# Kernel tuning notes

Measured on AMD Instinct MI355X. Metric: run time of the kernel, lower is better.

The kernel has to match this reference:

```python
import jax, jax.numpy as jnp
import numpy as np

B, S, Nv, D, DF, H = 8, 1024, 768, 512, 2048, 8
DH = D // H
EPS = 1e-5


def _layernorm(x, g, b):
    mu = jnp.mean(x, axis=-1, keepdims=True)
    var = jnp.mean((x - mu) ** 2, axis=-1, keepdims=True)
    return (x - mu) * jax.lax.rsqrt(var + EPS) * g + b


def _mha(x, Wq, Wk, Wv, Wo):
    b, s, d = x.shape
    q = (x @ Wq).reshape(b, s, H, DH)
    k = (x @ Wk).reshape(b, s, H, DH)
    v = (x @ Wv).reshape(b, s, H, DH)
    scores = jnp.einsum('bqhd,bkhd->bhqk', q, k) / np.sqrt(DH).astype(np.float32)
    a = jax.nn.softmax(scores, axis=-1)
    o = jnp.einsum('bhqk,bkhd->bqhd', a, v).reshape(b, s, d)
    return o @ Wo


def setup_inputs() -> dict:
    key = jax.random.key(0)
    ks = jax.random.split(key, 20)
    sc = 1.0 / np.sqrt(D)
    scf = 1.0 / np.sqrt(DF)
    n = lambda k, shp, s: (jax.random.normal(k, shp, jnp.float32) * s)
    return {
        'x': n(ks[0], (B, S, D), 1.0),
        'idx_emb_1': jax.random.randint(ks[1], (B, Nv), 0, Nv, dtype=jnp.int64) if jax.config.jax_enable_x64 else jax.random.randint(ks[1], (B, Nv), 0, Nv).astype(jnp.int32),
        'idx_pro_1': jax.random.randint(ks[2], (B, Nv), 0, Nv).astype(jnp.int32),
        'N': Nv,
        'Wq1': n(ks[3], (D, D), sc), 'Wk1': n(ks[4], (D, D), sc),
        'Wv1': n(ks[5], (D, D), sc), 'Wo1': n(ks[6], (D, D), sc),
        'Wq2': n(ks[7], (D, D), sc), 'Wk2': n(ks[8], (D, D), sc),
        'Wv2': n(ks[9], (D, D), sc), 'Wo2': n(ks[10], (D, D), sc),
        'w_conv1': n(ks[11], (D, DF), sc), 'b_conv1': jnp.zeros((DF,), jnp.float32),
        'w_conv2': n(ks[12], (DF, D), scf), 'b_conv2': jnp.zeros((D,), jnp.float32),
        'g1': jnp.ones((D,), jnp.float32), 'beta1': jnp.zeros((D,), jnp.float32),
        'g2': jnp.ones((D,), jnp.float32), 'beta2': jnp.zeros((D,), jnp.float32),
    }


def reference(x, idx_emb_1, idx_pro_1, N,
              Wq1, Wk1, Wv1, Wo1, Wq2, Wk2, Wv2, Wo2,
              w_conv1, b_conv1, w_conv2, b_conv2, g1, beta1, g2, beta2):
    # batched gather-reorder of first N tokens; rest pass through
    x_l1 = x.at[:, :N].set(jnp.take_along_axis(x[:, :N], idx_emb_1[:, :, None].astype(jnp.int32), axis=1))
    attn1 = _mha(x_l1, Wq1, Wk1, Wv1, Wo1)
    attn2 = jnp.flip(_mha(jnp.flip(x_l1, axis=1), Wq2, Wk2, Wv2, Wo2), axis=1)
    new_x1 = attn1 + attn2
    x_l2 = new_x1.at[:, :N].set(jnp.take_along_axis(new_x1[:, :N], idx_pro_1[:, :, None].astype(jnp.int32), axis=1))
    x = _layernorm(x + x_l2, g1, beta1)
    # kernel-size-1 Conv1d FFN == pointwise linear (dropout=0, eval mode)
    y = jnp.maximum(x @ w_conv1 + b_conv1, 0.0)
    y = y @ w_conv2 + b_conv2
    out = _layernorm(x + y, g2, beta2)
    return (out, attn1, attn2)
```

## Files before the change

kernel.cpp:

```cpp
#include <hip/hip_runtime.h>
#include <hip/hip_bf16.h>
#include <stdint.h>

#define B_ 8
#define S_ 1024
#define NV_ 768
#define D_ 512
#define DF_ 2048
#define H_ 8
#define DH_ 64
#define BS_ (B_*S_)
#define BSD_ ((size_t)B_*S_*D_)
#define QKVLD 3072

typedef __bf16 bf16x8 __attribute__((ext_vector_type(8)));
typedef __bf16 bf16x4v __attribute__((ext_vector_type(4)));
typedef float f32x4 __attribute__((ext_vector_type(4)));
typedef float f32x16 __attribute__((ext_vector_type(16)));
typedef __hip_bfloat16 bf16;

__device__ __forceinline__ void async_copy16(const void* g, void* l) {
  __builtin_amdgcn_global_load_lds((const __attribute__((address_space(1))) void*)g,
                                   (__attribute__((address_space(3))) void*)l, 16, 0, 0);
}

__device__ __forceinline__ void stage_tile(const bf16* __restrict__ g, int gRow0, long ldg,
                                           int gCol0, bf16* lds, int rows, int tid) {
  const int totalBytes = rows << 7;
  for (int off = tid * 16; off < totalBytes; off += 4096) {
    const int r = off >> 7;
    const int c = off & 127;
    const int srcByte = c ^ ((r & 7) << 4);
    const bf16* gp = g + (long)(gRow0 + r) * ldg + gCol0 + (srcByte >> 1);
    async_copy16(gp, (char*)lds + off);
  }
}

__device__ __forceinline__ bf16x8 lds_frag(const bf16* base, int row, int kElem) {
  const int byte = (row << 7) + ((kElem << 1) ^ ((row & 7) << 4));
  return *(const bf16x8*)((const char*)base + byte);
}

__device__ __forceinline__ bf16x8 v_frag(const bf16* base, int row, int c0) {
  const char* p = (const char*)base + (row << 7);
  const int swz = (row & 7) << 4;
  union { bf16x4v v[2]; bf16x8 b; } r;
  r.v[0] = *(const bf16x4v*)(p + (((c0) << 1) ^ swz));
  r.v[1] = *(const bf16x4v*)(p + (((c0 + 8) << 1) ^ swz));
  return r.b;
}

template<int BASE>
__device__ __forceinline__ bf16x8 p_frag(const f32x16& s) {
  union { ushort u[8]; bf16x8 b; } r;
#pragma unroll
  for (int e = 0; e < 8; e++)
    r.u[e] = __bfloat16_as_ushort(__float2bfloat16(s[BASE + e]));
  return r.b;
}

__device__ __forceinline__ f32x16 zero16() {
  f32x16 z;
#pragma unroll
  for (int i = 0; i < 16; i++) z[i] = 0.f;
  return z;
}

struct WP8 { const float* p[8]; };
__global__ __launch_bounds__(256) void wtrans8_kernel(WP8 ws, bf16* __restrict__ dstBase) {
  __shared__ float tile[32][33];
  const int z = blockIdx.z;
  const float sc = (z == 0 || z == 3) ? 0.1803368801f : 1.f;
  const float* __restrict__ src = ws.p[z];
  bf16* __restrict__ dst = dstBase + (size_t)z * D_ * D_;
  const int tx = threadIdx.x, ty = threadIdx.y;
  const int n0 = blockIdx.x * 32, k0 = blockIdx.y * 32;
#pragma unroll
  for (int i = 0; i < 4; i++) tile[ty + i * 8][tx] = src[(long)(k0 + ty + i * 8) * D_ + n0 + tx];
  __syncthreads();
#pragma unroll
  for (int i = 0; i < 4; i++)
    dst[(long)(n0 + ty + i * 8) * D_ + k0 + tx] = __float2bfloat16(tile[tx][ty + i * 8] * sc);
}

__global__ __launch_bounds__(256) void wtrans_kernel(const float* __restrict__ src,
                                                     bf16* __restrict__ dst, int K, int N) {
  __shared__ float tile[32][33];
  const int tx = threadIdx.x, ty = threadIdx.y;
  const int n0 = blockIdx.x * 32, k0 = blockIdx.y * 32;
#pragma unroll
  for (int i = 0; i < 4; i++) tile[ty + i * 8][tx] = src[(long)(k0 + ty + i * 8) * N + n0 + tx];
  __syncthreads();
#pragma unroll
  for (int i = 0; i < 4; i++)
    dst[(long)(n0 + ty + i * 8) * K + k0 + tx] = __float2bfloat16(tile[tx][ty + i * 8]);
}

__global__ __launch_bounds__(256) void vtrans_kernel(const bf16* __restrict__ qkv,
                                                     bf16* __restrict__ vtb) {
  __shared__ bf16 tile[32][33];
  const int tx = threadIdx.x, ty = threadIdx.y;
  const int s0 = blockIdx.x * 32, d0 = blockIdx.y * 32;
  const int z = blockIdx.z;
  const int set = z >> 6, bh = z & 63;
  const bf16* sp = qkv + (long)(bh >> 3) * S_ * QKVLD + set * 1536 + 1024 + (bh & 7) * 64;
  bf16* dp = vtb + (long)z * DH_ * S_;
#pragma unroll
  for (int i = 0; i < 4; i++) tile[ty + i * 8][tx] = sp[(long)(s0 + ty + i * 8) * QKVLD + d0 + tx];
  __syncthreads();
#pragma unroll
  for (int i = 0; i < 4; i++) dp[(long)(d0 + ty + i * 8) * S_ + s0 + tx] = tile[tx][ty + i * 8];
}

__global__ __launch_bounds__(256) void gather_cvt_kernel(const float* __restrict__ x,
                                                         const int* __restrict__ idx,
                                                         const int* __restrict__ Np,
                                                         bf16* __restrict__ out) {
  const int N = *Np;
  const int row = blockIdx.x * 2 + (threadIdx.x >> 7);
  const int t = threadIdx.x & 127;
  const int b = row >> 10, s = row & 1023;
  const int src = (s < N) ? idx[b * NV_ + s] : s;
  const float4 v = *(const float4*)(x + ((long)b * S_ + src) * D_ + t * 4);
  ushort4 u;
  u.x = (ushort)__bfloat16_as_ushort(__float2bfloat16(v.x));
  u.y = (ushort)__bfloat16_as_ushort(__float2bfloat16(v.y));
  u.z = (ushort)__bfloat16_as_ushort(__float2bfloat16(v.z));
  u.w = (ushort)__bfloat16_as_ushort(__float2bfloat16(v.w));
  *(ushort4*)(out + (long)row * D_ + t * 4) = u;
}

template<int BM, int BN, int MR, int NR, int OUTF, int BIAS, int RELU>
__global__ __launch_bounds__(256) void gemm_bt(const bf16* __restrict__ A, long lda, long sAz,
                                               const bf16* __restrict__ Bt, long sBz,
                                               const float* __restrict__ bias,
                                               void* __restrict__ C, long ldc, long sCz,
                                               int K) {
  constexpr int WC = BN / (NR * 16);
  constexpr int WR = BM / (MR * 16);
  static_assert(WR * WC == 4, "4 waves");
  __shared__ bf16 As[BM * 64];
  __shared__ bf16 Bs[BN * 64];
  const int tid = threadIdx.x;
  const int lane = tid & 63, wave = tid >> 6;
  const int wr = wave / WC, wc = wave % WC;
  const int g = lane >> 4, lr = lane & 15;
  const int m0 = blockIdx.x * BM, n0 = blockIdx.y * BN;
  const int z = blockIdx.z;
  A += (long)z * sAz;
  Bt += (long)z * sBz;

  f32x4 acc[MR][NR];
#pragma unroll
  for (int m = 0; m < MR; m++)
#pragma unroll
    for (int n = 0; n < NR; n++) acc[m][n] = (f32x4){0.f, 0.f, 0.f, 0.f};

  for (int kt = 0; kt < K; kt += 64) {
    stage_tile(A, m0, lda, kt, As, BM, tid);
    stage_tile(Bt, n0, K, kt, Bs, BN, tid);
    __syncthreads();
#pragma unroll
    for (int ks = 0; ks < 64; ks += 32) {
      const int kk = ks + g * 8;
      bf16x8 aF[MR], bF[NR];
#pragma unroll
      for (int m = 0; m < MR; m++) aF[m] = lds_frag(As, wr * (MR * 16) + m * 16 + lr, kk);
#pragma unroll
      for (int n = 0; n < NR; n++) bF[n] = lds_frag(Bs, wc * (NR * 16) + n * 16 + lr, kk);
#pragma unroll
      for (int m = 0; m < MR; m++)
#pragma unroll
        for (int n = 0; n < NR; n++)
          acc[m][n] = __builtin_amdgcn_mfma_f32_16x16x32_bf16(aF[m], bF[n], acc[m][n], 0, 0, 0);
    }
    __syncthreads();
  }

#pragma unroll
  for (int m = 0; m < MR; m++) {
#pragma unroll
    for (int n = 0; n < NR; n++) {
      const int row = m0 + wr * (MR * 16) + m * 16 + g * 4;
      const int col = n0 + wc * (NR * 16) + n * 16 + lr;
      const float bv = BIAS ? bias[col] : 0.f;
#pragma unroll
      for (int r = 0; r < 4; r++) {
        float v = acc[m][n][r] + bv;
        if (RELU) v = fmaxf(v, 0.f);
        if (OUTF) ((float*)C)[(long)z * sCz + (long)(row + r) * ldc + col] = v;
        else ((bf16*)C)[(long)z * sCz + (long)(row + r) * ldc + col] = __float2bfloat16(v);
      }
    }
  }
}

__global__ __launch_bounds__(256, 4) void flash_kernel(bf16* __restrict__ qkv,
                                                       const bf16* __restrict__ vtb) {
  __shared__ bf16 Qs[128 * 64];
  __shared__ bf16 Ks[64 * 64];
  __shared__ bf16 Vs[64 * 64];
  const int tid = threadIdx.x;
  const int lane = tid & 63, warp = tid >> 6;
  const int qlo = lane & 31, hi = lane >> 5;

  const int bid = (int)blockIdx.x;
  const int swz = (bid & 7) * 128 + (bid >> 3);
  const int qt = swz & 7;
  const int sbh = swz >> 3;
  const int set = sbh >> 6;
  const int b = (sbh >> 3) & 7, h = sbh & 7;

  bf16* Qp = qkv + (long)b * S_ * QKVLD + set * 1536 + h * DH_;
  const bf16* Kp = Qp + 512;
  const bf16* Vp = vtb + (long)sbh * DH_ * S_;

  stage_tile(Qp, qt * 128, QKVLD, 0, Qs, 128, tid);
  stage_tile(Kp, 0, QKVLD, 0, Ks, 64, tid);
  stage_tile(Vp, 0, S_, 0, Vs, 64, tid);
  __syncthreads();

  bf16x8 qFh[4];
#pragma unroll
  for (int d4 = 0; d4 < 4; d4++) qFh[d4] = lds_frag(Qs, warp * 32 + qlo, d4 * 16 + hi * 8);

  f32x16 oAcc0 = zero16(), oAcc1 = zero16();
  float mrun = -INFINITY, lrun = 0.f;

  for (int kt0 = 0; kt0 < S_; kt0 += 64) {
    f32x16 s0 = zero16(), s1 = zero16();
    __builtin_amdgcn_s_setprio(1);
#pragma unroll
    for (int d4 = 0; d4 < 4; d4++) {
      const int kc = d4 * 16 + hi * 8;
      bf16x8 kF0 = lds_frag(Ks, qlo, kc);
      bf16x8 kF1 = lds_frag(Ks, 32 + qlo, kc);
      s0 = __builtin_amdgcn_mfma_f32_32x32x16_bf16(kF0, qFh[d4], s0, 0, 0, 0);
      s1 = __builtin_amdgcn_mfma_f32_32x32x16_bf16(kF1, qFh[d4], s1, 0, 0, 0);
    }
    __builtin_amdgcn_s_setprio(0);

    float mx = s0[0];
#pragma unroll
    for (int r = 1; r < 16; r++) mx = fmaxf(mx, s0[r]);
#pragma unroll
    for (int r = 0; r < 16; r++) mx = fmaxf(mx, s1[r]);
    mx = fmaxf(mx, __shfl_xor(mx, 32, 64));

    if (!__all(mx - mrun <= 11.5f)) {
      const float mnew = fmaxf(mrun, mx);
      const float resc = exp2f(mrun - mnew);
      mrun = mnew;
      lrun *= resc;
#pragma unroll
      for (int r = 0; r < 16; r++) {
        const float rs = __shfl(resc, (r & 3) + 8 * (r >> 2) + 4 * hi, 64);
        oAcc0[r] *= rs;
        oAcc1[r] *= rs;
      }
    }

#pragma unroll
    for (int r = 0; r < 16; r++) s0[r] = exp2f(s0[r] - mrun);
#pragma unroll
    for (int r = 0; r < 16; r++) s1[r] = exp2f(s1[r] - mrun);

    float sm = 0.f;
#pragma unroll
    for (int r = 0; r < 16; r++) sm += s0[r] + s1[r];
    lrun += sm + __shfl_xor(sm, 32, 64);

    __builtin_amdgcn_s_setprio(1);
    {
      const bf16x8 pa0 = p_frag<0>(s0);
      oAcc0 = __builtin_amdgcn_mfma_f32_32x32x16_bf16(pa0, v_frag(Vs, qlo, 4 * hi), oAcc0, 0, 0, 0);
      oAcc1 = __builtin_amdgcn_mfma_f32_32x32x16_bf16(pa0, v_frag(Vs, 32 + qlo, 4 * hi), oAcc1, 0, 0, 0);
      const bf16x8 pa1 = p_frag<8>(s0);
      oAcc0 = __builtin_amdgcn_mfma_f32_32x32x16_bf16(pa1, v_frag(Vs, qlo, 16 + 4 * hi), oAcc0, 0, 0, 0);
      oAcc1 = __builtin_amdgcn_mfma_f32_32x32x16_bf16(pa1, v_frag(Vs, 32 + qlo, 16 + 4 * hi), oAcc1, 0, 0, 0);
      const bf16x8 pa2 = p_frag<0>(s1);
      oAcc0 = __builtin_amdgcn_mfma_f32_32x32x16_bf16(pa2, v_frag(Vs, qlo, 32 + 4 * hi), oAcc0, 0, 0, 0);
      oAcc1 = __builtin_amdgcn_mfma_f32_32x32x16_bf16(pa2, v_frag(Vs, 32 + qlo, 32 + 4 * hi), oAcc1, 0, 0, 0);
      const bf16x8 pa3 = p_frag<8>(s1);
      oAcc0 = __builtin_amdgcn_mfma_f32_32x32x16_bf16(pa3, v_frag(Vs, qlo, 48 + 4 * hi), oAcc0, 0, 0, 0);
      oAcc1 = __builtin_amdgcn_mfma_f32_32x32x16_bf16(pa3, v_frag(Vs, 32 + qlo, 48 + 4 * hi), oAcc1, 0, 0, 0);
    }
    __builtin_amdgcn_s_setprio(0);

    __syncthreads();
    if (kt0 + 64 < S_) {
      stage_tile(Kp, kt0 + 64, QKVLD, 0, Ks, 64, tid);
      stage_tile(Vp, 0, S_, kt0 + 64, Vs, 64, tid);
    }
    __syncthreads();
  }

#pragma unroll
  for (int r = 0; r < 16; r++) {
    const int q = (r & 3) + 8 * (r >> 2) + 4 * hi;
    const float linv = 1.f / __shfl(lrun, q, 64);
    bf16* op = Qp + (long)(qt * 128 + warp * 32 + q) * QKVLD;
    op[qlo] = __float2bfloat16(oAcc0[r] * linv);
    op[32 + qlo] = __float2bfloat16(oAcc1[r] * linv);
  }
}

__global__ __launch_bounds__(256) void fuse1_kernel(const float* __restrict__ x,
                                                    const float* __restrict__ a1,
                                                    const float* __restrict__ a2,
                                                    const int* __restrict__ idx,
                                                    const int* __restrict__ Np,
                                                    const float* __restrict__ gw,
                                                    const float* __restrict__ bw,
                                                    bf16* __restrict__ xlnB) {
  const int N = *Np;
  const int row = blockIdx.x * 4 + (threadIdx.x >> 6);
  const int lane = threadIdx.x & 63;
  const int b = row >> 10, s = row & 1023;
  const int j = (s < N) ? idx[b * NV_ + s] : s;
  const float* xp = x + (long)row * D_ + lane * 8;
  const float* p1 = a1 + ((long)b * S_ + j) * D_ + lane * 8;
  const float* p2 = a2 + ((long)b * S_ + j) * D_ + lane * 8;
  float v[8];
  float sum = 0.f;
#pragma unroll
  for (int q = 0; q < 2; q++) {
    const float4 t = ((const float4*)xp)[q];
    const float4 u = ((const float4*)p1)[q];
    const float4 w = ((const float4*)p2)[q];
    v[q * 4 + 0] = t.x + u.x + w.x; v[q * 4 + 1] = t.y + u.y + w.y;
    v[q * 4 + 2] = t.z + u.z + w.z; v[q * 4 + 3] = t.w + u.w + w.w;
  }
#pragma unroll
  for (int i = 0; i < 8; i++) sum += v[i];
#pragma unroll
  for (int o = 1; o < 64; o <<= 1) sum += __shfl_xor(sum, o, 64);
  const float mu = sum * (1.f / D_);
  float var = 0.f;
#pragma unroll
  for (int i = 0; i < 8; i++) { const float t = v[i] - mu; var += t * t; }
#pragma unroll
  for (int o = 1; o < 64; o <<= 1) var += __shfl_xor(var, o, 64);
  const float rs = rsqrtf(var * (1.f / D_) + 1e-5f);
#pragma unroll
  for (int i = 0; i < 8; i++) {
    const int d = lane * 8 + i;
    xlnB[(long)row * D_ + d] = __float2bfloat16((v[i] - mu) * rs * gw[d] + bw[d]);
  }
}

__global__ __launch_bounds__(256) void fuse2_kernel(const bf16* __restrict__ xlnB,
                                                    const bf16* __restrict__ ybf,
                                                    const float* __restrict__ gw,
                                                    const float* __restrict__ bw,
                                                    float* __restrict__ out) {
  const int row = blockIdx.x * 4 + (threadIdx.x >> 6);
  const int lane = threadIdx.x & 63;
  const bf16* xp = xlnB + (long)row * D_ + lane * 8;
  const bf16* yp = ybf + (long)row * D_ + lane * 8;
  float v[8];
  float sum = 0.f;
#pragma unroll
  for (int i = 0; i < 8; i++) {
    v[i] = __bfloat162float(xp[i]) + __bfloat162float(yp[i]);
    sum += v[i];
  }
#pragma unroll
  for (int o = 1; o < 64; o <<= 1) sum += __shfl_xor(sum, o, 64);
  const float mu = sum * (1.f / D_);
  float var = 0.f;
#pragma unroll
  for (int i = 0; i < 8; i++) { const float t = v[i] - mu; var += t * t; }
#pragma unroll
  for (int o = 1; o < 64; o <<= 1) var += __shfl_xor(var, o, 64);
  const float rs = rsqrtf(var * (1.f / D_) + 1e-5f);
#pragma unroll
  for (int i = 0; i < 8; i++) {
    const int d = lane * 8 + i;
    out[(long)row * D_ + d] = (v[i] - mu) * rs * gw[d] + bw[d];
  }
}

extern "C" void kernel_launch(void* const* d_in, const int* in_sizes, int n_in,
                              void* d_out, int out_size, void* d_ws, size_t ws_size,
                              hipStream_t stream) {
  const float* x   = (const float*)d_in[0];
  const int* idx1  = (const int*)d_in[1];
  const int* idx2  = (const int*)d_in[2];
  const int* Np    = (const int*)d_in[3];
  const float* b_conv1 = (const float*)d_in[13];
  const float* b_conv2 = (const float*)d_in[15];
  const float* g1    = (const float*)d_in[16];
  const float* beta1 = (const float*)d_in[17];
  const float* g2    = (const float*)d_in[18];
  const float* beta2 = (const float*)d_in[19];

  float* outp  = (float*)d_out;
  float* attn1 = outp + BSD_;

  const size_t DD = (size_t)D_ * D_;
  char* w = (char*)d_ws;
  bf16* wT  = (bf16*)w;
  bf16* w1T = wT + 8 * DD;
  bf16* w2T = w1T + (size_t)DF_ * D_;
  bf16* qkv = (bf16*)(w + (8ll << 20));
  bf16* xl1 = (bf16*)(w + (56ll << 20));
  bf16* vtb = (bf16*)(w + (56ll << 20));
  bf16* xlnB = (bf16*)(w + (56ll << 20));
  bf16* ffn = (bf16*)(w + (8ll << 20));
  bf16* ybf = (bf16*)(w + (40ll << 20));

  WP8 wp;
  wp.p[0] = (const float*)d_in[4];
  wp.p[1] = (const float*)d_in[5];
  wp.p[2] = (const float*)d_in[6];
  wp.p[3] = (const float*)d_in[8];
  wp.p[4] = (const float*)d_in[9];
  wp.p[5] = (const float*)d_in[10];
  wp.p[6] = (const float*)d_in[7];
  wp.p[7] = (const float*)d_in[11];

  const dim3 tb(32, 8);
  wtrans8_kernel<<<dim3(16, 16, 8), tb, 0, stream>>>(wp, wT);
  wtrans_kernel<<<dim3(DF_ / 32, D_ / 32), tb, 0, stream>>>((const float*)d_in[12], w1T, D_, DF_);
  wtrans_kernel<<<dim3(D_ / 32, DF_ / 32), tb, 0, stream>>>((const float*)d_in[14], w2T, DF_, D_);

  gather_cvt_kernel<<<BS_ / 2, 256, 0, stream>>>(x, idx1, Np, xl1);

  gemm_bt<128, 128, 4, 4, 0, 0, 0><<<dim3(BS_ / 128, QKVLD / 128, 1), 256, 0, stream>>>(
      xl1, D_, 0, wT, 0, nullptr, qkv, QKVLD, 0, D_);

  vtrans_kernel<<<dim3(S_ / 32, DH_ / 32, 128), tb, 0, stream>>>(qkv, vtb);

  flash_kernel<<<1024, 256, 0, stream>>>(qkv, vtb);

  gemm_bt<128, 64, 4, 2, 1, 0, 0><<<dim3(BS_ / 128, D_ / 64, 2), 256, 0, stream>>>(
      qkv, QKVLD, 1536, wT + 6 * DD, (long)DD, nullptr, attn1, D_, (long)BSD_, D_);

  fuse1_kernel<<<BS_ / 4, 256, 0, stream>>>(x, attn1, attn1 + BSD_, idx2, Np, g1, beta1, xlnB);

  gemm_bt<128, 128, 4, 4, 0, 1, 1><<<dim3(BS_ / 128, DF_ / 128, 1), 256, 0, stream>>>(
      xlnB, D_, 0, w1T, 0, b_conv1, ffn, DF_, 0, D_);
  gemm_bt<128, 64, 4, 2, 0, 1, 0><<<dim3(BS_ / 128, D_ / 64, 1), 256, 0, stream>>>(
      ffn, DF_, 0, w2T, 0, b_conv2, ybf, D_, 0, DF_);

  fuse2_kernel<<<BS_ / 4, 256, 0, stream>>>(xlnB, ybf, g2, beta2, outp);
}
```

Baseline: 217.3 us.

## Double-buffer K/V in flash attention, pre-permute V, compute row sums with MFMA

```diff
diff --git a/kernel.cpp b/kernel.cpp
--- a/kernel.cpp
+++ b/kernel.cpp
@@ -14,7 +14,6 @@
 #define QKVLD 3072
 
 typedef __bf16 bf16x8 __attribute__((ext_vector_type(8)));
-typedef __bf16 bf16x4v __attribute__((ext_vector_type(4)));
 typedef float f32x4 __attribute__((ext_vector_type(4)));
 typedef float f32x16 __attribute__((ext_vector_type(16)));
 typedef __hip_bfloat16 bf16;
@@ -41,21 +40,19 @@
   return *(const bf16x8*)((const char*)base + byte);
 }
 
-__device__ __forceinline__ bf16x8 v_frag(const bf16* base, int row, int c0) {
-  const char* p = (const char*)base + (row << 7);
-  const int swz = (row & 7) << 4;
-  union { bf16x4v v[2]; bf16x8 b; } r;
-  r.v[0] = *(const bf16x4v*)(p + (((c0) << 1) ^ swz));
-  r.v[1] = *(const bf16x4v*)(p + (((c0 + 8) << 1) ^ swz));
-  return r.b;
-}
-
 template<int BASE>
 __device__ __forceinline__ bf16x8 p_frag(const f32x16& s) {
   union { ushort u[8]; bf16x8 b; } r;
 #pragma unroll
   for (int e = 0; e < 8; e++)
     r.u[e] = __bfloat16_as_ushort(__float2bfloat16(s[BASE + e]));
+  return r.b;
+}
+
+__device__ __forceinline__ bf16x8 ones_frag() {
+  union { ushort u[8]; bf16x8 b; } r;
+#pragma unroll
+  for (int e = 0; e < 8; e++) r.u[e] = 0x3F80;
   return r.b;
 }
 
@@ -108,8 +105,10 @@
 #pragma unroll
   for (int i = 0; i < 4; i++) tile[ty + i * 8][tx] = sp[(long)(s0 + ty + i * 8) * QKVLD + d0 + tx];
   __syncthreads();
-#pragma unroll
-  for (int i = 0; i < 4; i++) dp[(long)(d0 + ty + i * 8) * S_ + s0 + tx] = tile[tx][ty + i * 8];
+  const int c = s0 + tx;
+  const int cp = (c & ~12) | ((c & 4) << 1) | ((c & 8) >> 1);
+#pragma unroll
+  for (int i = 0; i < 4; i++) dp[(long)(d0 + ty + i * 8) * S_ + cp] = tile[tx][ty + i * 8];
 }
 
 __global__ __launch_bounds__(256) void gather_cvt_kernel(const float* __restrict__ x,
@@ -197,9 +196,7 @@
 
 __global__ __launch_bounds__(256, 4) void flash_kernel(bf16* __restrict__ qkv,
                                                        const bf16* __restrict__ vtb) {
-  __shared__ bf16 Qs[128 * 64];
-  __shared__ bf16 Ks[64 * 64];
-  __shared__ bf16 Vs[64 * 64];
+  __shared__ char lds[32768];
   const int tid = threadIdx.x;
   const int lane = tid & 63, warp = tid >> 6;
   const int qlo = lane & 31, hi = lane >> 5;
@@ -215,34 +212,44 @@
   const bf16* Kp = Qp + 512;
   const bf16* Vp = vtb + (long)sbh * DH_ * S_;
 
-  stage_tile(Qp, qt * 128, QKVLD, 0, Qs, 128, tid);
-  stage_tile(Kp, 0, QKVLD, 0, Ks, 64, tid);
-  stage_tile(Vp, 0, S_, 0, Vs, 64, tid);
+  bf16* const buf0 = (bf16*)(lds + 16384);
+  bf16* const buf1 = (bf16*)lds;
+
+  stage_tile(Qp, qt * 128, QKVLD, 0, (bf16*)lds, 128, tid);
+  stage_tile(Kp, 0, QKVLD, 0, buf0, 64, tid);
+  stage_tile(Vp, 0, S_, 0, buf0 + 4096, 64, tid);
   __syncthreads();
 
   bf16x8 qFh[4];
 #pragma unroll
-  for (int d4 = 0; d4 < 4; d4++) qFh[d4] = lds_frag(Qs, warp * 32 + qlo, d4 * 16 + hi * 8);
-
-  f32x16 oAcc0 = zero16(), oAcc1 = zero16();
-  float mrun = -INFINITY, lrun = 0.f;
-
-  for (int kt0 = 0; kt0 < S_; kt0 += 64) {
+  for (int d4 = 0; d4 < 4; d4++)
+    qFh[d4] = lds_frag((bf16*)lds, warp * 32 + qlo, d4 * 16 + hi * 8);
+  __syncthreads();
+
+  stage_tile(Kp, 64, QKVLD, 0, buf1, 64, tid);
+  stage_tile(Vp, 0, S_, 64, buf1 + 4096, 64, tid);
+
+  f32x16 oAcc0 = zero16(), oAcc1 = zero16(), sAcc = zero16();
+  float mrun = -INFINITY;
+  const bf16x8 onesF = ones_frag();
+
+  for (int t = 0; t < 16; t++) {
+    bf16* const Kb = (t & 1) ? buf1 : buf0;
+    bf16* const Vb = Kb + 4096;
+
     f32x16 s0 = zero16(), s1 = zero16();
     __builtin_amdgcn_s_setprio(1);
 #pragma unroll
     for (int d4 = 0; d4 < 4; d4++) {
       const int kc = d4 * 16 + hi * 8;
-      bf16x8 kF0 = lds_frag(Ks, qlo, kc);
-      bf16x8 kF1 = lds_frag(Ks, 32 + qlo, kc);
-      s0 = __builtin_amdgcn_mfma_f32_32x32x16_bf16(kF0, qFh[d4], s0, 0, 0, 0);
-      s1 = __builtin_amdgcn_mfma_f32_32x32x16_bf16(kF1, qFh[d4], s1, 0, 0, 0);
+      s0 = __builtin_amdgcn_mfma_f32_32x32x16_bf16(lds_frag(Kb, qlo, kc), qFh[d4], s0, 0, 0, 0);
+      s1 = __builtin_amdgcn_mfma_f32_32x32x16_bf16(lds_frag(Kb, 32 + qlo, kc), qFh[d4], s1, 0, 0, 0);
     }
     __builtin_amdgcn_s_setprio(0);
 
-    float mx = s0[0];
-#pragma unroll
-    for (int r = 1; r < 16; r++) mx = fmaxf(mx, s0[r]);
+    float mx = fmaxf(s0[0], s0[1]);
+#pragma unroll
+    for (int r = 2; r < 16; r++) mx = fmaxf(mx, s0[r]);
 #pragma unroll
     for (int r = 0; r < 16; r++) mx = fmaxf(mx, s1[r]);
     mx = fmaxf(mx, __shfl_xor(mx, 32, 64));
@@ -251,12 +258,12 @@
       const float mnew = fmaxf(mrun, mx);
       const float resc = exp2f(mrun - mnew);
       mrun = mnew;
-      lrun *= resc;
 #pragma unroll
       for (int r = 0; r < 16; r++) {
         const float rs = __shfl(resc, (r & 3) + 8 * (r >> 2) + 4 * hi, 64);
         oAcc0[r] *= rs;
         oAcc1[r] *= rs;
+        sAcc[r] *= rs;
       }
     }
 
@@ -264,41 +271,39 @@
     for (int r = 0; r < 16; r++) s0[r] = exp2f(s0[r] - mrun);
 #pragma unroll
     for (int r = 0; r < 16; r++) s1[r] = exp2f(s1[r] - mrun);
-
-    float sm = 0.f;
-#pragma unroll
-    for (int r = 0; r < 16; r++) sm += s0[r] + s1[r];
-    lrun += sm + __shfl_xor(sm, 32, 64);
 
     __builtin_amdgcn_s_setprio(1);
     {
       const bf16x8 pa0 = p_frag<0>(s0);
-      oAcc0 = __builtin_amdgcn_mfma_f32_32x32x16_bf16(pa0, v_frag(Vs, qlo, 4 * hi), oAcc0, 0, 0, 0);
-      oAcc1 = __builtin_amdgcn_mfma_f32_32x32x16_bf16(pa0, v_frag(Vs, 32 + qlo, 4 * hi), oAcc1, 0, 0, 0);
+      oAcc0 = __builtin_amdgcn_mfma_f32_32x32x16_bf16(pa0, lds_frag(Vb, qlo, hi * 8), oAcc0, 0, 0, 0);
+      oAcc1 = __builtin_amdgcn_mfma_f32_32x32x16_bf16(pa0, lds_frag(Vb, 32 + qlo, hi * 8), oAcc1, 0, 0, 0);
+      sAcc = __builtin_amdgcn_mfma_f32_32x32x16_bf16(pa0, onesF, sAcc, 0, 0, 0);
       const bf16x8 pa1 = p_frag<8>(s0);
-      oAcc0 = __builtin_amdgcn_mfma_f32_32x32x16_bf16(pa1, v_frag(Vs, qlo, 16 + 4 * hi), oAcc0, 0, 0, 0);
-      oAcc1 = __builtin_amdgcn_mfma_f32_32x32x16_bf16(pa1, v_frag(Vs, 32 + qlo, 16 + 4 * hi), oAcc1, 0, 0, 0);
+      oAcc0 = __builtin_amdgcn_mfma_f32_32x32x16_bf16(pa1, lds_frag(Vb, qlo, 16 + hi * 8), oAcc0, 0, 0, 0);
+      oAcc1 = __builtin_amdgcn_mfma_f32_32x32x16_bf16(pa1, lds_frag(Vb, 32 + qlo, 16 + hi * 8), oAcc1, 0, 0, 0);
+      sAcc = __builtin_amdgcn_mfma_f32_32x32x16_bf16(pa1, onesF, sAcc, 0, 0, 0);
       const bf16x8 pa2 = p_frag<0>(s1);
-      oAcc0 = __builtin_amdgcn_mfma_f32_32x32x16_bf16(pa2, v_frag(Vs, qlo, 32 + 4 * hi), oAcc0, 0, 0, 0);
-      oAcc1 = __builtin_amdgcn_mfma_f32_32x32x16_bf16(pa2, v_frag(Vs, 32 + qlo, 32 + 4 * hi), oAcc1, 0, 0, 0);
+      oAcc0 = __builtin_amdgcn_mfma_f32_32x32x16_bf16(pa2, lds_frag(Vb, qlo, 32 + hi * 8), oAcc0, 0, 0, 0);
+      oAcc1 = __builtin_amdgcn_mfma_f32_32x32x16_bf16(pa2, lds_frag(Vb, 32 + qlo, 32 + hi * 8), oAcc1, 0, 0, 0);
+      sAcc = __builtin_amdgcn_mfma_f32_32x32x16_bf16(pa2, onesF, sAcc, 0, 0, 0);
       const bf16x8 pa3 = p_frag<8>(s1);
-      oAcc0 = __builtin_amdgcn_mfma_f32_32x32x16_bf16(pa3, v_frag(Vs, qlo, 48 + 4 * hi), oAcc0, 0, 0, 0);
-      oAcc1 = __builtin_amdgcn_mfma_f32_32x32x16_bf16(pa3, v_frag(Vs, 32 + qlo, 48 + 4 * hi), oAcc1, 0, 0, 0);
+      oAcc0 = __builtin_amdgcn_mfma_f32_32x32x16_bf16(pa3, lds_frag(Vb, qlo, 48 + hi * 8), oAcc0, 0, 0, 0);
+      oAcc1 = __builtin_amdgcn_mfma_f32_32x32x16_bf16(pa3, lds_frag(Vb, 32 + qlo, 48 + hi * 8), oAcc1, 0, 0, 0);
+      sAcc = __builtin_amdgcn_mfma_f32_32x32x16_bf16(pa3, onesF, sAcc, 0, 0, 0);
     }
     __builtin_amdgcn_s_setprio(0);
 
     __syncthreads();
-    if (kt0 + 64 < S_) {
-      stage_tile(Kp, kt0 + 64, QKVLD, 0, Ks, 64, tid);
-      stage_tile(Vp, 0, S_, kt0 + 64, Vs, 64, tid);
-    }
-    __syncthreads();
+    if (t + 2 < 16) {
+      stage_tile(Kp, (t + 2) * 64, QKVLD, 0, Kb, 64, tid);
+      stage_tile(Vp, 0, S_, (t + 2) * 64, Kb + 4096, 64, tid);
+    }
   }
 
 #pragma unroll
   for (int r = 0; r < 16; r++) {
     const int q = (r & 3) + 8 * (r >> 2) + 4 * hi;
-    const float linv = 1.f / __shfl(lrun, q, 64);
+    const float linv = 1.f / sAcc[r];
     bf16* op = Qp + (long)(qt * 128 + warp * 32 + q) * QKVLD;
     op[qlo] = __float2bfloat16(oAcc0[r] * linv);
     op[32 + qlo] = __float2bfloat16(oAcc1[r] * linv);
```

Result: no change. 218.4 us (+0.5%).
